# Optimization experiments

Hardware: AMD Instinct MI355X
Metric: run time of the kernel (lower is better)

Reference implementation:

```python
import jax, jax.numpy as jnp
import numpy as np

N = 50000      # nodes
F = 128        # feature_dim
H = 128        # hidden_dim
E = 1_600_000  # edges
G = 64         # graphs in batch
A = 8          # n_actions


def setup_inputs() -> dict:
    key = jax.random.key(0)
    ks = jax.random.split(key, 12)
    s = 0.05
    return {
        "x": jax.random.normal(ks[0], (N, F), jnp.float32),
        "edge_attr": jax.random.uniform(ks[1], (E, 1), jnp.float32),
        "W_e1": jax.random.normal(ks[2], (3, 1), jnp.float32) * s,
        "b_e1": jnp.zeros((1,), jnp.float32),
        "W_e2": jax.random.normal(ks[3], (1, 1), jnp.float32) * s,
        "b_e2": jnp.zeros((1,), jnp.float32),
        "W_gcn": jax.random.normal(ks[4], (F, H), jnp.float32) * s,
        "b_gcn": jnp.zeros((H,), jnp.float32),
        "W2": jax.random.normal(ks[5], (H, H), jnp.float32) * s,
        "b2": jnp.zeros((H,), jnp.float32),
        "W3": jax.random.normal(ks[6], (H, A), jnp.float32) * s,
        "b3": jnp.zeros((A,), jnp.float32),
        "edge_index": jax.random.randint(ks[7], (2, E), 0, N, jnp.int64),
        "batch": jnp.sort(jax.random.randint(ks[8], (N,), 0, G, jnp.int64)),
    }


def reference(x, edge_attr, W_e1, b_e1, W_e2, b_e2, W_gcn, b_gcn, W2, b2, W3, b3, edge_index, batch):
    # edge MLP: input is [src, dst, edge_attr] per edge -> (E, 3)
    e_feat = jnp.concatenate([edge_index.T.astype(x.dtype), edge_attr], axis=1)
    h = jax.nn.relu(e_feat @ W_e1 + b_e1)
    w = jax.nn.sigmoid(h @ W_e2 + b_e2)[:, 0]  # (E,)

    # GCNConv: add self-loops (weight 1), symmetric normalization
    loop = jnp.arange(N)
    row = jnp.concatenate([edge_index[0], loop])      # source
    col = jnp.concatenate([edge_index[1], loop])      # target
    w_all = jnp.concatenate([w, jnp.ones((N,), w.dtype)])
    deg = jax.ops.segment_sum(w_all, col, num_segments=N)
    safe_deg = jnp.where(deg > 0, deg, 1.0)
    dis = jnp.where(deg > 0, 1.0 / jnp.sqrt(safe_deg), 0.0)  # deg^-1/2, inf->0
    norm = dis[row] * w_all * dis[col]                # (E+N,)

    xw = x @ W_gcn                                    # (N, H)
    msg = norm[:, None] * xw[row]                     # (E+N, H) gather
    conv = jax.ops.segment_sum(msg, col, num_segments=N) + b_gcn  # scatter
    h1 = jax.nn.relu(conv)

    # global_mean_pool over batch index
    sums = jax.ops.segment_sum(h1, batch, num_segments=G)
    cnt = jax.ops.segment_sum(jnp.ones((N,), h1.dtype), batch, num_segments=G)
    pooled = sums / jnp.maximum(cnt, 1.0)[:, None]    # (G, H)

    h2 = jax.nn.relu(pooled @ W2 + b2)
    return h2 @ W3 + b3                               # (G, A)
```

## Files before the change

kernel.cpp:

```cpp
#include <hip/hip_runtime.h>
#include <hip/hip_fp16.h>
#include <math.h>

#define GB 64
#define AD 8
#define NC2 256
#define BSH 6
#define BS  64
#define NBMAX 1024

typedef _Float16 half8 __attribute__((ext_vector_type(8)));
typedef float    f32x4 __attribute__((ext_vector_type(4)));

__global__ __launch_bounds__(512) void k_hist2(const int* __restrict__ ei,
                                               int* __restrict__ H2,
                                               int E, int ce, int NB) {
    __shared__ int h[NBMAX];
    int c = blockIdx.x;
    for (int b = threadIdx.x; b < NB; b += 512) h[b] = 0;
    __syncthreads();
    int e0 = c * ce, e1 = min(e0 + ce, E);
    int nv = (e1 - e0) & ~3;
    const int4* dst4 = (const int4*)(ei + E + e0);
    for (int v = threadIdx.x; v < (nv >> 2); v += 512) {
        int4 d = dst4[v];
        atomicAdd(&h[d.x >> BSH], 1);
        atomicAdd(&h[d.y >> BSH], 1);
        atomicAdd(&h[d.z >> BSH], 1);
        atomicAdd(&h[d.w >> BSH], 1);
    }
    for (int e = e0 + nv + threadIdx.x; e < e1; e += 512)
        atomicAdd(&h[ei[E + e] >> BSH], 1);
    __syncthreads();
    for (int b = threadIdx.x; b < NB; b += 512)
        H2[(size_t)c * NB + b] = h[b];
}

__global__ __launch_bounds__(256) void k_cscan(int* __restrict__ H2,
                                               int* __restrict__ cntB,
                                               int NB, int nc) {
    __shared__ int ssum[256];
    int b = blockIdx.x;
    int t = threadIdx.x;
    int v = (t < nc) ? H2[(size_t)t * NB + b] : 0;
    ssum[t] = v;
    __syncthreads();
    for (int s = 1; s < 256; s <<= 1) {
        int tmp = (t >= s) ? ssum[t - s] : 0;
        __syncthreads();
        ssum[t] += tmp;
        __syncthreads();
    }
    if (t < nc) H2[(size_t)t * NB + b] = ssum[t] - v;
    if (t == 255) cntB[b] = ssum[255];
}

__global__ __launch_bounds__(1024) void k_bscan(const int* __restrict__ cntB,
                                                int* __restrict__ bb,
                                                int* __restrict__ rowptr,
                                                float* __restrict__ psum,
                                                int NB, int n, int E) {
    __shared__ int sm[1024];
    int t = threadIdx.x;
    for (int z = t; z < GB * 128 + GB; z += 1024) psum[z] = 0.0f;
    int v = (t < NB) ? cntB[t] : 0;
    sm[t] = v;
    __syncthreads();
    for (int s = 1; s < 1024; s <<= 1) {
        int tmp = (t >= s) ? sm[t - s] : 0;
        __syncthreads();
        sm[t] += tmp;
        __syncthreads();
    }
    if (t < NB) bb[t] = sm[t] - v;
    if (t == NB - 1) bb[NB] = sm[t];
    if (t == 0) rowptr[n] = E;
}

__global__ __launch_bounds__(512) void k_fill2(const int* __restrict__ ei,
                                               const float* __restrict__ attr,
                                               const float* __restrict__ W_e1,
                                               const float* __restrict__ b_e1,
                                               const float* __restrict__ W_e2,
                                               const float* __restrict__ b_e2,
                                               const int* __restrict__ bb,
                                               const int* __restrict__ H2,
                                               int2* __restrict__ rec,
                                               int E, int ce, int NB) {
    __shared__ int off[NBMAX];
    int c = blockIdx.x;
    for (int b = threadIdx.x; b < NB; b += 512)
        off[b] = bb[b] + H2[(size_t)c * NB + b];
    __syncthreads();
    float w1s = W_e1[0], w1d = W_e1[1], w1a = W_e1[2], bb1 = b_e1[0];
    float w2 = W_e2[0], bb2 = b_e2[0];
    int e0 = c * ce, e1 = min(e0 + ce, E);
    int nv = (e1 - e0) & ~3;
    const int4*   src4 = (const int4*)(ei + e0);
    const int4*   dst4 = (const int4*)(ei + E + e0);
    const float4* att4 = (const float4*)(attr + e0);
    for (int v = threadIdx.x; v < (nv >> 2); v += 512) {
        int4 sv = src4[v];
        int4 dv = dst4[v];
        float4 av = att4[v];
        int   ss[4] = {sv.x, sv.y, sv.z, sv.w};
        int   dd[4] = {dv.x, dv.y, dv.z, dv.w};
        float aa[4] = {av.x, av.y, av.z, av.w};
        #pragma unroll
        for (int k = 0; k < 4; k++) {
            float h = fmaxf((float)ss[k] * w1s + (float)dd[k] * w1d + aa[k] * w1a + bb1, 0.0f);
            float w = 1.0f / (1.0f + expf(-(h * w2 + bb2)));
            int pos = atomicAdd(&off[dd[k] >> BSH], 1);
            int2 rv;
            rv.x = ss[k] | ((dd[k] & (BS - 1)) << 16);
            rv.y = __float_as_int(w);
            rec[pos] = rv;
        }
    }
    for (int e = e0 + nv + threadIdx.x; e < e1; e += 512) {
        int d = ei[E + e];
        int s = ei[e];
        float h = fmaxf((float)s * w1s + (float)d * w1d + attr[e] * w1a + bb1, 0.0f);
        float w = 1.0f / (1.0f + expf(-(h * w2 + bb2)));
        int pos = atomicAdd(&off[d >> BSH], 1);
        int2 rv;
        rv.x = s | ((d & (BS - 1)) << 16);
        rv.y = __float_as_int(w);
        rec[pos] = rv;
    }
}

__global__ __launch_bounds__(256) void k_bucket(const int2* __restrict__ rec,
                                                const int* __restrict__ bb,
                                                unsigned int* __restrict__ rec3,
                                                int* __restrict__ rowptr,
                                                float* __restrict__ dis, int n) {
    __shared__ int   cntL[BS];
    __shared__ float degL[BS];
    __shared__ int   pfx[BS];
    __shared__ int   cnt2[BS];
    int b = blockIdx.x;
    int t = threadIdx.x;
    if (t < BS) { cntL[t] = 0; degL[t] = 1.0f; cnt2[t] = 0; }
    __syncthreads();
    int s0 = bb[b], s1 = bb[b + 1];
    for (int j = s0 + t; j < s1; j += 256) {
        int2 rv = rec[j];
        int dl = (rv.x >> 16) & (BS - 1);
        atomicAdd(&cntL[dl], 1);
        atomicAdd(&degL[dl], __int_as_float(rv.y));
    }
    __syncthreads();
    if (t == 0) {
        int acc = 0;
        for (int k = 0; k < BS; k++) { pfx[k] = acc; acc += cntL[k]; }
    }
    __syncthreads();
    int lo = b << BSH;
    if (t < BS) {
        int i = lo + t;
        if (i < n) {
            rowptr[i] = s0 + pfx[t];
            dis[i] = rsqrtf(degL[t]);
        }
    }
    for (int j = s0 + t; j < s1; j += 256) {
        int2 rv = rec[j];
        int dl = (rv.x >> 16) & (BS - 1);
        int r = atomicAdd(&cnt2[dl], 1);
        unsigned int hh = (unsigned int)__half_as_ushort(
                              __float2half(__int_as_float(rv.y)));
        rec3[s0 + pfx[dl] + r] = (unsigned int)(rv.x & 0xFFFF) | (hh << 16);
    }
}

__global__ __launch_bounds__(256) void k_xw(const float* __restrict__ x,
                                            const float* __restrict__ Wg,
                                            const float* __restrict__ dis,
                                            __half* __restrict__ xwh, int n) {
    __shared__ _Float16 Wh[128 * 136];
    int tid = threadIdx.x;
    for (int idx = tid; idx < 128 * 128; idx += 256) {
        int k = idx >> 7, c = idx & 127;
        Wh[c * 136 + k] = (_Float16)Wg[idx];
    }
    __syncthreads();

    int lane = tid & 63;
    int w = tid >> 6;
    int n16 = lane & 15;
    int quad = lane >> 4;

    #pragma unroll
    for (int hf = 0; hf < 2; hf++) {
        int r0 = blockIdx.x * 128 + hf * 64 + w * 16;
        if (r0 >= n) break;
        int arow = min(r0 + n16, n - 1);
        const float* xrow = x + (size_t)arow * 128;

        f32x4 acc[8];
        #pragma unroll
        for (int nt = 0; nt < 8; nt++) acc[nt] = (f32x4){0.f, 0.f, 0.f, 0.f};

        #pragma unroll
        for (int kk = 0; kk < 4; kk++) {
            int k0 = kk * 32 + quad * 8;
            float4 f0 = *(const float4*)(xrow + k0);
            float4 f1 = *(const float4*)(xrow + k0 + 4);
            half8 a;
            a[0] = (_Float16)f0.x; a[1] = (_Float16)f0.y;
            a[2] = (_Float16)f0.z; a[3] = (_Float16)f0.w;
            a[4] = (_Float16)f1.x; a[5] = (_Float16)f1.y;
            a[6] = (_Float16)f1.z; a[7] = (_Float16)f1.w;
            #pragma unroll
            for (int nt = 0; nt < 8; nt++) {
                half8 b = *(const half8*)&Wh[(nt * 16 + n16) * 136 + k0];
                acc[nt] = __builtin_amdgcn_mfma_f32_16x16x32_f16(a, b, acc[nt], 0, 0, 0);
            }
        }

        #pragma unroll
        for (int r = 0; r < 4; r++) {
            int row = r0 + quad * 4 + r;
            if (row < n) {
                float dv = dis[row];
                #pragma unroll
                for (int nt = 0; nt < 8; nt++)
                    xwh[(size_t)row * 128 + nt * 16 + n16] = __float2half(acc[nt][r] * dv);
            }
        }
    }
}

__global__ __launch_bounds__(256) void k_gather(const unsigned int* __restrict__ rec3,
                                                const int* __restrict__ rowptr,
                                                const float* __restrict__ dis,
                                                const __half* __restrict__ xh,
                                                const float* __restrict__ bg,
                                                __half* __restrict__ conv, int n) {
    int wave = threadIdx.x >> 6;
    int lane = threadIdx.x & 63;
    int g = lane >> 4;
    int q = lane & 15;
    int i = blockIdx.x * 4 + wave;
    if (i >= n) return;
    int st = rowptr[i];
    int m = rowptr[i + 1] - st;
    float di = dis[i];
    float acc[8];
    {
        uint4 sr = *(const uint4*)(xh + (size_t)i * 128 + q * 8);
        const __half2* hp = (const __half2*)&sr;
        float sc = (g == 0) ? 1.0f : 0.0f;
        #pragma unroll
        for (int k = 0; k < 4; k++) {
            float2 f = __half22float2(hp[k]);
            acc[2 * k]     = sc * f.x;
            acc[2 * k + 1] = sc * f.y;
        }
    }
    for (int base = 0; base < m; base += 64) {
        int kk = min(64, m - base);
        unsigned int rv = 0u;
        if (lane < kk) rv = rec3[st + base + lane];
        int jn = (kk + 3) >> 2;
        #pragma unroll 8
        for (int j = 0; j < jn; j++) {
            unsigned int rvj = (unsigned int)__builtin_amdgcn_ds_bpermute(
                                   ((j << 2) + g) << 2, (int)rv);
            int s = rvj & 0xFFFF;
            float cf = __half2float(__ushort_as_half((unsigned short)(rvj >> 16)));
            uint4 rw = *(const uint4*)(xh + (size_t)s * 128 + q * 8);
            const __half2* rp = (const __half2*)&rw;
            #pragma unroll
            for (int k = 0; k < 4; k++) {
                float2 f = __half22float2(rp[k]);
                acc[2 * k]     += cf * f.x;
                acc[2 * k + 1] += cf * f.y;
            }
        }
    }
    #pragma unroll
    for (int k = 0; k < 8; k++) {
        acc[k] += __shfl_xor(acc[k], 16);
        acc[k] += __shfl_xor(acc[k], 32);
    }
    if (g == 0) {
        float4 b0 = *(const float4*)(bg + q * 8);
        float4 b1 = *(const float4*)(bg + q * 8 + 4);
        const float* bp = (const float*)&b0;
        float v[8];
        #pragma unroll
        for (int k = 0; k < 4; k++) v[k] = fmaxf(di * acc[k] + bp[k], 0.0f);
        bp = (const float*)&b1;
        #pragma unroll
        for (int k = 0; k < 4; k++) v[4 + k] = fmaxf(di * acc[4 + k] + bp[k], 0.0f);
        __half2 h[4];
        #pragma unroll
        for (int k = 0; k < 4; k++)
            h[k] = __halves2half2(__float2half(v[2 * k]), __float2half(v[2 * k + 1]));
        uint4 o;
        o.x = *(unsigned int*)&h[0];
        o.y = *(unsigned int*)&h[1];
        o.z = *(unsigned int*)&h[2];
        o.w = *(unsigned int*)&h[3];
        *(uint4*)(conv + (size_t)i * 128 + q * 8) = o;
    }
}

__device__ __forceinline__ int lbound(const int* __restrict__ a, int n, int v) {
    int lo = 0, hi = n;
    while (lo < hi) {
        int mid = (lo + hi) >> 1;
        if (a[mid] < v) lo = mid + 1; else hi = mid;
    }
    return lo;
}

__global__ __launch_bounds__(256) void k_pool(const __half* __restrict__ h1,
                                              const int* __restrict__ batch,
                                              float* __restrict__ psum,
                                              float* __restrict__ pcnt, int n) {
    int g = blockIdx.x, ch = blockIdx.y;
    int t = threadIdx.x;
    int s = lbound(batch, n, g);
    int e = lbound(batch, n, g + 1);
    int rq = t >> 6, q = t & 63;
    float ax = 0.0f, ay = 0.0f;
    for (int i = s + ch * 4 + rq; i < e; i += 16) {
        __half2 hv = *(const __half2*)(h1 + (size_t)i * 128 + 2 * q);
        float2 f = __half22float2(hv);
        ax += f.x; ay += f.y;
    }
    __shared__ float2 sm[256];
    sm[t] = make_float2(ax, ay);
    __syncthreads();
    if (t < 64) {
        float2 a0 = sm[t], a1 = sm[t + 64], a2 = sm[t + 128], a3 = sm[t + 192];
        atomicAdd(&psum[g * 128 + 2 * q],     a0.x + a1.x + a2.x + a3.x);
        atomicAdd(&psum[g * 128 + 2 * q + 1], a0.y + a1.y + a2.y + a3.y);
    }
    if (ch == 0 && t == 0) pcnt[g] = (float)(e - s);
}

__global__ __launch_bounds__(128) void k_head(const float* __restrict__ psum,
                                              const float* __restrict__ pcnt,
                                              const float* __restrict__ W2,
                                              const float* __restrict__ b2,
                                              const float* __restrict__ W3,
                                              const float* __restrict__ b3,
                                              float* __restrict__ out) {
    __shared__ float pl[128];
    __shared__ float h2s[128];
    int g = blockIdx.x;
    int t = threadIdx.x;
    float c = fmaxf(pcnt[g], 1.0f);
    pl[t] = psum[g * 128 + t] / c;
    __syncthreads();
    float acc = b2[t];
    for (int k = 0; k < 128; k++) acc += pl[k] * W2[k * 128 + t];
    h2s[t] = fmaxf(acc, 0.0f);
    __syncthreads();
    if (t < AD) {
        float o = b3[t];
        for (int k = 0; k < 128; k++) o += h2s[k] * W3[k * AD + t];
        out[g * AD + t] = o;
    }
}

extern "C" void kernel_launch(void* const* d_in, const int* in_sizes, int n_in,
                              void* d_out, int out_size, void* d_ws, size_t ws_size,
                              hipStream_t stream) {
    const float* x        = (const float*)d_in[0];
    const float* edge_attr= (const float*)d_in[1];
    const float* W_e1     = (const float*)d_in[2];
    const float* b_e1     = (const float*)d_in[3];
    const float* W_e2     = (const float*)d_in[4];
    const float* b_e2     = (const float*)d_in[5];
    const float* W_gcn    = (const float*)d_in[6];
    const float* b_gcn    = (const float*)d_in[7];
    const float* W2       = (const float*)d_in[8];
    const float* b2       = (const float*)d_in[9];
    const float* W3       = (const float*)d_in[10];
    const float* b3       = (const float*)d_in[11];
    const int*   ei       = (const int*)d_in[12];
    const int*   batch    = (const int*)d_in[13];
    float* out = (float*)d_out;

    const int E  = in_sizes[12] / 2;
    const int n  = in_sizes[13];
    const int NB = (n + BS - 1) >> BSH;
    const int ce = (((E + NC2 - 1) / NC2) + 3) & ~3;

    char* p = (char*)d_ws;
    __half* xwh   = (__half*)p;  p += (size_t)n * 128 * sizeof(__half);
    int*    H2    = (int*)p;
    __half* conv  = (__half*)p;  p += (size_t)n * 128 * sizeof(__half);
    int2*   rec   = (int2*)p;    p += (size_t)E * sizeof(int2);
    unsigned int* rec3 = (unsigned int*)p; p += (size_t)E * sizeof(unsigned int);
    float*  dis   = (float*)p;   p += (size_t)n * sizeof(float);
    float*  psum  = (float*)p;   p += (size_t)GB * 128 * sizeof(float);
    float*  pcnt  = (float*)p;   p += (size_t)GB * sizeof(float);
    int*    rowptr= (int*)p;     p += (size_t)(n + 1) * sizeof(int);
    int*    cntB  = (int*)p;     p += (size_t)NBMAX * sizeof(int);
    int*    bb    = (int*)p;     p += (size_t)(NBMAX + 1) * sizeof(int);

    k_hist2<<<NC2, 512, 0, stream>>>(ei, H2, E, ce, NB);
    k_cscan<<<NB, 256, 0, stream>>>(H2, cntB, NB, NC2);
    k_bscan<<<1, 1024, 0, stream>>>(cntB, bb, rowptr, psum, NB, n, E);
    k_fill2<<<NC2, 512, 0, stream>>>(ei, edge_attr, W_e1, b_e1, W_e2, b_e2,
                                     bb, H2, rec, E, ce, NB);
    k_bucket<<<NB, 256, 0, stream>>>(rec, bb, rec3, rowptr, dis, n);
    k_xw<<<(n + 127) / 128, 256, 0, stream>>>(x, W_gcn, dis, xwh, n);
    k_gather<<<(n + 3) / 4, 256, 0, stream>>>(rec3, rowptr, dis, xwh,
                                              b_gcn, conv, n);
    k_pool<<<dim3(GB, 4), 256, 0, stream>>>(conv, batch, psum, pcnt, n);
    k_head<<<GB, 128, 0, stream>>>(psum, pcnt, W2, b2, W3, b3, out);
}
```

Measured before the change: 237.3 us.

## Fuse mean-pool into gather via per-block atomics and batch neighbor loads

New measurement: 232.0 us. -2.2%, faster.

```diff
diff --git a/kernel.cpp b/kernel.cpp
--- a/kernel.cpp
+++ b/kernel.cpp
@@ -62,7 +62,7 @@
                                                 int NB, int n, int E) {
     __shared__ int sm[1024];
     int t = threadIdx.x;
-    for (int z = t; z < GB * 128 + GB; z += 1024) psum[z] = 0.0f;
+    for (int z = t; z < GB * 128; z += 1024) psum[z] = 0.0f;
     int v = (t < NB) ? cntB[t] : 0;
     sm[t] = v;
     __syncthreads();
@@ -237,18 +237,27 @@
                                                 const float* __restrict__ dis,
                                                 const __half* __restrict__ xh,
                                                 const float* __restrict__ bg,
-                                                __half* __restrict__ conv, int n) {
+                                                const int* __restrict__ batch,
+                                                float* __restrict__ psum, int n) {
+    __shared__ float ps4[4][128];
+    __shared__ int   gix[4];
     int wave = threadIdx.x >> 6;
     int lane = threadIdx.x & 63;
     int g = lane >> 4;
     int q = lane & 15;
     int i = blockIdx.x * 4 + wave;
-    if (i >= n) return;
-    int st = rowptr[i];
-    int m = rowptr[i + 1] - st;
-    float di = dis[i];
+    bool valid = (i < n);
+
+    int st = 0, m = 0;
+    float di = 0.0f;
     float acc[8];
-    {
+    #pragma unroll
+    for (int k = 0; k < 8; k++) acc[k] = 0.0f;
+
+    if (valid) {
+        st = rowptr[i];
+        m = rowptr[i + 1] - st;
+        di = dis[i];
         uint4 sr = *(const uint4*)(xh + (size_t)i * 128 + q * 8);
         const __half2* hp = (const __half2*)&sr;
         float sc = (g == 0) ? 1.0f : 0.0f;
@@ -258,53 +267,68 @@
             acc[2 * k]     = sc * f.x;
             acc[2 * k + 1] = sc * f.y;
         }
-    }
-    for (int base = 0; base < m; base += 64) {
-        int kk = min(64, m - base);
-        unsigned int rv = 0u;
-        if (lane < kk) rv = rec3[st + base + lane];
-        int jn = (kk + 3) >> 2;
-        #pragma unroll 8
-        for (int j = 0; j < jn; j++) {
-            unsigned int rvj = (unsigned int)__builtin_amdgcn_ds_bpermute(
-                                   ((j << 2) + g) << 2, (int)rv);
-            int s = rvj & 0xFFFF;
-            float cf = __half2float(__ushort_as_half((unsigned short)(rvj >> 16)));
-            uint4 rw = *(const uint4*)(xh + (size_t)s * 128 + q * 8);
-            const __half2* rp = (const __half2*)&rw;
-            #pragma unroll
-            for (int k = 0; k < 4; k++) {
-                float2 f = __half22float2(rp[k]);
-                acc[2 * k]     += cf * f.x;
-                acc[2 * k + 1] += cf * f.y;
+        for (int base = 0; base < m; base += 64) {
+            int kk = min(64, m - base);
+            unsigned int rv = 0u;
+            if (lane < kk) rv = rec3[st + base + lane];
+            int jn = (kk + 3) >> 2;
+            for (int j = 0; j < jn; j += 8) {
+                float cf[8];
+                uint4 rw[8];
+                #pragma unroll
+                for (int u = 0; u < 8; u++) {
+                    int idx = ((j + u) << 2) + g;
+                    unsigned int rvj = (unsigned int)__builtin_amdgcn_ds_bpermute(
+                                           idx << 2, (int)rv);
+                    int s = rvj & 0xFFFF;
+                    cf[u] = __half2float(__ushort_as_half((unsigned short)(rvj >> 16)));
+                    rw[u] = *(const uint4*)(xh + (size_t)s * 128 + q * 8);
+                }
+                #pragma unroll
+                for (int u = 0; u < 8; u++) {
+                    const __half2* rp = (const __half2*)&rw[u];
+                    #pragma unroll
+                    for (int k = 0; k < 4; k++) {
+                        float2 f = __half22float2(rp[k]);
+                        acc[2 * k]     += cf[u] * f.x;
+                        acc[2 * k + 1] += cf[u] * f.y;
+                    }
+                }
             }
         }
-    }
-    #pragma unroll
-    for (int k = 0; k < 8; k++) {
-        acc[k] += __shfl_xor(acc[k], 16);
-        acc[k] += __shfl_xor(acc[k], 32);
-    }
-    if (g == 0) {
+        #pragma unroll
+        for (int k = 0; k < 8; k++) {
+            acc[k] += __shfl_xor(acc[k], 16);
+            acc[k] += __shfl_xor(acc[k], 32);
+        }
+    }
+
+    if (lane == 0) gix[wave] = valid ? batch[i] : -1;
+    if (valid && g == 0) {
         float4 b0 = *(const float4*)(bg + q * 8);
         float4 b1 = *(const float4*)(bg + q * 8 + 4);
         const float* bp = (const float*)&b0;
-        float v[8];
-        #pragma unroll
-        for (int k = 0; k < 4; k++) v[k] = fmaxf(di * acc[k] + bp[k], 0.0f);
+        #pragma unroll
+        for (int k = 0; k < 4; k++)
+            ps4[wave][q * 8 + k] = fmaxf(di * acc[k] + bp[k], 0.0f);
         bp = (const float*)&b1;
         #pragma unroll
-        for (int k = 0; k < 4; k++) v[4 + k] = fmaxf(di * acc[4 + k] + bp[k], 0.0f);
-        __half2 h[4];
-        #pragma unroll
         for (int k = 0; k < 4; k++)
-            h[k] = __halves2half2(__float2half(v[2 * k]), __float2half(v[2 * k + 1]));
-        uint4 o;
-        o.x = *(unsigned int*)&h[0];
-        o.y = *(unsigned int*)&h[1];
-        o.z = *(unsigned int*)&h[2];
-        o.w = *(unsigned int*)&h[3];
-        *(uint4*)(conv + (size_t)i * 128 + q * 8) = o;
+            ps4[wave][q * 8 + 4 + k] = fmaxf(di * acc[4 + k] + bp[k], 0.0f);
+    }
+    __syncthreads();
+    int t = threadIdx.x;
+    if (t < 128) {
+        int g0 = gix[0];
+        if (g0 >= 0 && gix[1] == g0 && gix[2] == g0 && gix[3] == g0) {
+            float s = ps4[0][t] + ps4[1][t] + ps4[2][t] + ps4[3][t];
+            atomicAdd(&psum[g0 * 128 + t], s);
+        } else {
+            #pragma unroll
+            for (int w2 = 0; w2 < 4; w2++)
+                if (gix[w2] >= 0)
+                    atomicAdd(&psum[gix[w2] * 128 + t], ps4[w2][t]);
+        }
     }
 }
 
@@ -317,45 +341,25 @@
     return lo;
 }
 
-__global__ __launch_bounds__(256) void k_pool(const __half* __restrict__ h1,
+__global__ __launch_bounds__(128) void k_head(const float* __restrict__ psum,
                                               const int* __restrict__ batch,
-                                              float* __restrict__ psum,
-                                              float* __restrict__ pcnt, int n) {
-    int g = blockIdx.x, ch = blockIdx.y;
-    int t = threadIdx.x;
-    int s = lbound(batch, n, g);
-    int e = lbound(batch, n, g + 1);
-    int rq = t >> 6, q = t & 63;
-    float ax = 0.0f, ay = 0.0f;
-    for (int i = s + ch * 4 + rq; i < e; i += 16) {
-        __half2 hv = *(const __half2*)(h1 + (size_t)i * 128 + 2 * q);
-        float2 f = __half22float2(hv);
-        ax += f.x; ay += f.y;
-    }
-    __shared__ float2 sm[256];
-    sm[t] = make_float2(ax, ay);
-    __syncthreads();
-    if (t < 64) {
-        float2 a0 = sm[t], a1 = sm[t + 64], a2 = sm[t + 128], a3 = sm[t + 192];
-        atomicAdd(&psum[g * 128 + 2 * q],     a0.x + a1.x + a2.x + a3.x);
-        atomicAdd(&psum[g * 128 + 2 * q + 1], a0.y + a1.y + a2.y + a3.y);
-    }
-    if (ch == 0 && t == 0) pcnt[g] = (float)(e - s);
-}
-
-__global__ __launch_bounds__(128) void k_head(const float* __restrict__ psum,
-                                              const float* __restrict__ pcnt,
                                               const float* __restrict__ W2,
                                               const float* __restrict__ b2,
                                               const float* __restrict__ W3,
                                               const float* __restrict__ b3,
-                                              float* __restrict__ out) {
+                                              float* __restrict__ out, int n) {
     __shared__ float pl[128];
     __shared__ float h2s[128];
+    __shared__ float cS;
     int g = blockIdx.x;
     int t = threadIdx.x;
-    float c = fmaxf(pcnt[g], 1.0f);
-    pl[t] = psum[g * 128 + t] / c;
+    if (t == 0) {
+        int s = lbound(batch, n, g);
+        int e = lbound(batch, n, g + 1);
+        cS = fmaxf((float)(e - s), 1.0f);
+    }
+    __syncthreads();
+    pl[t] = psum[g * 128 + t] / cS;
     __syncthreads();
     float acc = b2[t];
     for (int k = 0; k < 128; k++) acc += pl[k] * W2[k * 128 + t];
@@ -394,8 +398,7 @@
 
     char* p = (char*)d_ws;
     __half* xwh   = (__half*)p;  p += (size_t)n * 128 * sizeof(__half);
-    int*    H2    = (int*)p;
-    __half* conv  = (__half*)p;  p += (size_t)n * 128 * sizeof(__half);
+    int*    H2    = (int*)p;     p += (size_t)n * 128 * sizeof(__half);
     int2*   rec   = (int2*)p;    p += (size_t)E * sizeof(int2);
     unsigned int* rec3 = (unsigned int*)p; p += (size_t)E * sizeof(unsigned int);
     float*  dis   = (float*)p;   p += (size_t)n * sizeof(float);
@@ -404,6 +407,7 @@
     int*    rowptr= (int*)p;     p += (size_t)(n + 1) * sizeof(int);
     int*    cntB  = (int*)p;     p += (size_t)NBMAX * sizeof(int);
     int*    bb    = (int*)p;     p += (size_t)(NBMAX + 1) * sizeof(int);
+    (void)pcnt;
 
     k_hist2<<<NC2, 512, 0, stream>>>(ei, H2, E, ce, NB);
     k_cscan<<<NB, 256, 0, stream>>>(H2, cntB, NB, NC2);
@@ -413,7 +417,6 @@
     k_bucket<<<NB, 256, 0, stream>>>(rec, bb, rec3, rowptr, dis, n);
     k_xw<<<(n + 127) / 128, 256, 0, stream>>>(x, W_gcn, dis, xwh, n);
     k_gather<<<(n + 3) / 4, 256, 0, stream>>>(rec3, rowptr, dis, xwh,
-                                              b_gcn, conv, n);
-    k_pool<<<dim3(GB, 4), 256, 0, stream>>>(conv, batch, psum, pcnt, n);
-    k_head<<<GB, 128, 0, stream>>>(psum, pcnt, W2, b2, W3, b3, out);
-}
+                                              b_gcn, batch, psum, n);
+    k_head<<<GB, 128, 0, stream>>>(psum, batch, W2, b2, W3, b3, out, n);
+}
```
